# Performance work log

Hardware: AMD Instinct MI355X
Metric: run time of the kernel (lower is better)

## Reference

```python
import jax, jax.numpy as jnp
import numpy as np

# Static configuration (mirrors the list of reconstruction_blocks)
B, F, D, H = 16384, 64, 32, 64
CARDS = ([4, 8, 16, 32] * 8) + [1] * 32  # 32 categorical + 32 numerical features
CMAX = max(CARDS)                         # pad all per-feature output dims to CMAX
TOTAL = sum(CARDS)                        # 512 = concat output width
# flat column indices selecting the valid (unpadded) outputs per feature
_flat = np.concatenate([np.arange(c) + f * CMAX for f, c in enumerate(CARDS)])
FLAT_IDX = jnp.asarray(_flat, dtype=jnp.int32)


def setup_inputs() -> dict:
    key = jax.random.key(0)
    k0, k1, k2 = jax.random.split(key, 3)
    return {
        "inputs": jax.random.normal(k0, (B, F, D), dtype=jnp.float32),
        # per-feature hidden layer: Dense(D -> H)
        "W1": jax.random.normal(k1, (F, D, H), dtype=jnp.float32) / np.float32(np.sqrt(D)),
        "b1": jnp.zeros((F, H), dtype=jnp.float32),
        # per-feature output layer, padded to CMAX columns (only CARDS[f] are used)
        "W2": jax.random.normal(k2, (F, H, CMAX), dtype=jnp.float32) / np.float32(np.sqrt(H)),
        "b2": jnp.zeros((F, CMAX), dtype=jnp.float32),
    }


def reference(inputs, W1, b1, W2, b2):
    # Batched grouped-GEMM over all per-feature MLP blocks at once.
    h = jax.nn.relu(jnp.einsum('bfd,fdh->bfh', inputs, W1) + b1)       # [B,F,H]
    out_pad = jnp.einsum('bfh,fhc->bfc', h, W2) + b2                   # [B,F,CMAX]
    # concat of per-feature outputs (varying widths) == gather of valid columns
    return out_pad.reshape(B, F * CMAX)[:, FLAT_IDX]                   # [B,TOTAL]
```

## Files before the change

### kernel.cpp

```cpp
#include <hip/hip_runtime.h>

typedef __attribute__((ext_vector_type(8))) short short8;
typedef __attribute__((ext_vector_type(4))) float f32x4;

#define DI __device__ __forceinline__

namespace {
constexpr int F_   = 64;
constexpr int D_   = 32;
constexpr int H_   = 64;
constexpr int CM_  = 32;
constexpr int TOT_ = 512;
constexpr int BT_  = 256;
constexpr int NB_  = (16384 / BT_) * F_;
}

DI unsigned short f2bf(float v) {
    __bf16 h = (__bf16)v;
    return __builtin_bit_cast(unsigned short, h);
}

__global__ __launch_bounds__(256)
void recon_kernel(const float* __restrict__ x, const float* __restrict__ W1,
                  const float* __restrict__ b1, const float* __restrict__ W2,
                  const float* __restrict__ b2, float* __restrict__ out)
{
    __shared__ __align__(16) unsigned short w1t[H_ * D_];
    __shared__ __align__(16) unsigned short w2t[CM_ * H_];
    __shared__ __align__(16) unsigned short hb[4][16 * H_];

    const int bid   = blockIdx.x;
    const int f     = (bid >> 3) & 63;
    const int btile = ((bid & 7) << 3) | (bid >> 9);

    const int tid  = threadIdx.x;
    const int lane = tid & 63;
    const int wv   = tid >> 6;
    const int l15  = lane & 15;
    const int kg   = lane >> 4;

    {
        const int e0 = tid * 8;
        const float* W1f = W1 + f * (D_ * H_);
        const float* W2f = W2 + f * (H_ * CM_);
        f32x4 v0 = *(const f32x4*)(W1f + e0);
        f32x4 v1 = *(const f32x4*)(W1f + e0 + 4);
        f32x4 u0 = *(const f32x4*)(W2f + e0);
        f32x4 u1 = *(const f32x4*)(W2f + e0 + 4);
#pragma unroll
        for (int j = 0; j < 8; ++j) {
            int e = e0 + j;
            float v = (j < 4) ? v0[j] : v1[j - 4];
            w1t[(e & 63) * D_ + (e >> 6)] = f2bf(v);
            float u = (j < 4) ? u0[j] : u1[j - 4];
            w2t[(e & 31) * H_ + (e >> 5)] = f2bf(u);
        }
    }
    __syncthreads();

    short8 w1b[4];
#pragma unroll
    for (int nt = 0; nt < 4; ++nt)
        w1b[nt] = *(const short8*)&w1t[(nt * 16 + l15) * D_ + kg * 8];

    short8 w2b[2][2];
#pragma unroll
    for (int nt = 0; nt < 2; ++nt)
#pragma unroll
        for (int ks = 0; ks < 2; ++ks)
            w2b[nt][ks] = *(const short8*)&w2t[(nt * 16 + l15) * H_ + ks * 32 + kg * 8];

    float b1v[4], b2v[2];
#pragma unroll
    for (int nt = 0; nt < 4; ++nt) b1v[nt] = b1[f * H_ + nt * 16 + l15];
#pragma unroll
    for (int nt = 0; nt < 2; ++nt) b2v[nt] = b2[f * CM_ + nt * 16 + l15];

    int card, off;
    if (f < 32) { card = 4 << (f & 3); off = (f >> 2) * 60 + card - 4; }
    else        { card = 1;            off = 480 + (f - 32); }

    unsigned short* hw = hb[wv];
    const f32x4 zero = {0.f, 0.f, 0.f, 0.f};
    const int b0 = btile * BT_ + wv * 64;

#pragma unroll
    for (int t = 0; t < 4; ++t) {
        const int rbase = b0 + t * 16;

        const float* xr = x + (size_t)(rbase + l15) * (F_ * D_) + f * D_ + kg * 8;
        f32x4 a0 = *(const f32x4*)xr;
        f32x4 a1 = *(const f32x4*)(xr + 4);
        short8 af;
#pragma unroll
        for (int j = 0; j < 4; ++j) {
            af[j]     = (short)f2bf(a0[j]);
            af[4 + j] = (short)f2bf(a1[j]);
        }

        f32x4 c1[4];
#pragma unroll
        for (int nt = 0; nt < 4; ++nt)
            c1[nt] = __builtin_amdgcn_mfma_f32_16x16x32_bf16(af, w1b[nt], zero, 0, 0, 0);

#pragma unroll
        for (int nt = 0; nt < 4; ++nt) {
#pragma unroll
            for (int j = 0; j < 4; ++j) {
                int r = kg * 4 + j;
                int c = nt * 16 + l15;
                float v = c1[nt][j] + b1v[nt];
                v = v > 0.f ? v : 0.f;
                int idx = (r * H_ + c) ^ ((r & 7) << 3);
                hw[idx] = f2bf(v);
            }
        }

        short8 ha[2];
#pragma unroll
        for (int ks = 0; ks < 2; ++ks) {
            int idx = (l15 * H_ + ks * 32 + kg * 8) ^ ((l15 & 7) << 3);
            ha[ks] = *(const short8*)&hw[idx];
        }

        f32x4 c2[2];
        c2[0] = __builtin_amdgcn_mfma_f32_16x16x32_bf16(ha[0], w2b[0][0], zero, 0, 0, 0);
        c2[0] = __builtin_amdgcn_mfma_f32_16x16x32_bf16(ha[1], w2b[0][1], c2[0], 0, 0, 0);
        if (card == 32) {
            c2[1] = __builtin_amdgcn_mfma_f32_16x16x32_bf16(ha[0], w2b[1][0], zero, 0, 0, 0);
            c2[1] = __builtin_amdgcn_mfma_f32_16x16x32_bf16(ha[1], w2b[1][1], c2[1], 0, 0, 0);
        }

        const int ntiles = (card == 32) ? 2 : 1;
        for (int nt = 0; nt < ntiles; ++nt) {
            int c = nt * 16 + l15;
            if (c < card) {
                float bias = b2v[nt];
#pragma unroll
                for (int j = 0; j < 4; ++j) {
                    int row = rbase + kg * 4 + j;
                    out[(size_t)row * TOT_ + off + c] = c2[nt][j] + bias;
                }
            }
        }
    }
}

extern "C" void kernel_launch(void* const* d_in, const int* in_sizes, int n_in,
                              void* d_out, int out_size, void* d_ws, size_t ws_size,
                              hipStream_t stream) {
    const float* x  = (const float*)d_in[0];
    const float* W1 = (const float*)d_in[1];
    const float* b1 = (const float*)d_in[2];
    const float* W2 = (const float*)d_in[3];
    const float* b2 = (const float*)d_in[4];
    float* out = (float*)d_out;
    recon_kernel<<<NB_, 256, 0, stream>>>(x, W1, b1, W2, b2, out);
}
```

Baseline: 39.83 us.

## Process eight features per block and stage outputs in LDS for coalesced stores

Each 512-thread block now handles a 64-row tile across eight features, one wave per feature, and loads W1/W2 for all eight into a shared buffer that is reused in phases. All x loads are issued before compute. Per-feature outputs, which are narrow and scattered, are written to an LDS staging tile and then stored to global memory as contiguous 16-byte row segments instead of scattered scalar stores. This aims to cut uncoalesced writes and raise load-level parallelism, at the cost of extra barriers, more LDS per block and fewer blocks.

```diff
diff --git a/kernel.cpp b/kernel.cpp
--- a/kernel.cpp
+++ b/kernel.cpp
@@ -6,13 +6,9 @@
 #define DI __device__ __forceinline__
 
 namespace {
-constexpr int F_   = 64;
-constexpr int D_   = 32;
-constexpr int H_   = 64;
-constexpr int CM_  = 32;
 constexpr int TOT_ = 512;
-constexpr int BT_  = 256;
-constexpr int NB_  = (16384 / BT_) * F_;
+constexpr int XROW = 2048;
+constexpr int NB_  = 2048;
 }
 
 DI unsigned short f2bf(float v) {
@@ -20,82 +16,102 @@
     return __builtin_bit_cast(unsigned short, h);
 }
 
-__global__ __launch_bounds__(256)
+__global__ __launch_bounds__(512)
 void recon_kernel(const float* __restrict__ x, const float* __restrict__ W1,
                   const float* __restrict__ b1, const float* __restrict__ W2,
                   const float* __restrict__ b2, float* __restrict__ out)
 {
-    __shared__ __align__(16) unsigned short w1t[H_ * D_];
-    __shared__ __align__(16) unsigned short w2t[CM_ * H_];
-    __shared__ __align__(16) unsigned short hb[4][16 * H_];
+    __shared__ __align__(16) unsigned short u_sm[24576];
 
-    const int bid   = blockIdx.x;
-    const int f     = (bid >> 3) & 63;
-    const int btile = ((bid & 7) << 3) | (bid >> 9);
+    const int bid     = blockIdx.x;
+    const int xcd     = bid & 7;
+    const int ii      = bid >> 3;
+    const int fg      = ii & 7;
+    const int rowtile = (xcd << 5) | (ii >> 3);
+    const int r0      = rowtile << 6;
 
     const int tid  = threadIdx.x;
     const int lane = tid & 63;
     const int wv   = tid >> 6;
     const int l15  = lane & 15;
     const int kg   = lane >> 4;
+    const int f    = fg * 8 + wv;
 
     {
-        const int e0 = tid * 8;
-        const float* W1f = W1 + f * (D_ * H_);
-        const float* W2f = W2 + f * (H_ * CM_);
-        f32x4 v0 = *(const f32x4*)(W1f + e0);
-        f32x4 v1 = *(const f32x4*)(W1f + e0 + 4);
-        f32x4 u0 = *(const f32x4*)(W2f + e0);
-        f32x4 u1 = *(const f32x4*)(W2f + e0 + 4);
+        const float* src = W1 + (size_t)fg * 8 * 2048;
 #pragma unroll
-        for (int j = 0; j < 8; ++j) {
-            int e = e0 + j;
-            float v = (j < 4) ? v0[j] : v1[j - 4];
-            w1t[(e & 63) * D_ + (e >> 6)] = f2bf(v);
-            float u = (j < 4) ? u0[j] : u1[j - 4];
-            w2t[(e & 31) * H_ + (e >> 5)] = f2bf(u);
+        for (int it = 0; it < 4; ++it) {
+            int e0 = (it * 512 + tid) * 8;
+            f32x4 v0 = *(const f32x4*)(src + e0);
+            f32x4 v1 = *(const f32x4*)(src + e0 + 4);
+#pragma unroll
+            for (int j = 0; j < 8; ++j) {
+                int e = e0 + j, f8 = e >> 11, r = e & 2047;
+                float v = (j < 4) ? v0[j] : v1[j - 4];
+                u_sm[(f8 << 11) | ((r & 63) << 5) | (r >> 6)] = f2bf(v);
+            }
         }
     }
     __syncthreads();
-
     short8 w1b[4];
 #pragma unroll
     for (int nt = 0; nt < 4; ++nt)
-        w1b[nt] = *(const short8*)&w1t[(nt * 16 + l15) * D_ + kg * 8];
+        w1b[nt] = *(const short8*)&u_sm[wv * 2048 + (nt * 16 + l15) * 32 + kg * 8];
+    __syncthreads();
 
+    {
+        const float* src = W2 + (size_t)fg * 8 * 2048;
+#pragma unroll
+        for (int it = 0; it < 4; ++it) {
+            int e0 = (it * 512 + tid) * 8;
+            f32x4 v0 = *(const f32x4*)(src + e0);
+            f32x4 v1 = *(const f32x4*)(src + e0 + 4);
+#pragma unroll
+            for (int j = 0; j < 8; ++j) {
+                int e = e0 + j, f8 = e >> 11, r = e & 2047;
+                float v = (j < 4) ? v0[j] : v1[j - 4];
+                u_sm[(f8 << 11) | ((r & 31) << 6) | (r >> 5)] = f2bf(v);
+            }
+        }
+    }
+    __syncthreads();
     short8 w2b[2][2];
 #pragma unroll
     for (int nt = 0; nt < 2; ++nt)
 #pragma unroll
         for (int ks = 0; ks < 2; ++ks)
-            w2b[nt][ks] = *(const short8*)&w2t[(nt * 16 + l15) * H_ + ks * 32 + kg * 8];
+            w2b[nt][ks] = *(const short8*)&u_sm[wv * 2048 + (nt * 16 + l15) * 64 + ks * 32 + kg * 8];
+    __syncthreads();
 
     float b1v[4], b2v[2];
 #pragma unroll
-    for (int nt = 0; nt < 4; ++nt) b1v[nt] = b1[f * H_ + nt * 16 + l15];
+    for (int nt = 0; nt < 4; ++nt) b1v[nt] = b1[f * 64 + nt * 16 + l15];
 #pragma unroll
-    for (int nt = 0; nt < 2; ++nt) b2v[nt] = b2[f * CM_ + nt * 16 + l15];
+    for (int nt = 0; nt < 2; ++nt) b2v[nt] = b2[f * 32 + nt * 16 + l15];
 
-    int card, off;
-    if (f < 32) { card = 4 << (f & 3); off = (f >> 2) * 60 + card - 4; }
-    else        { card = 1;            off = 480 + (f - 32); }
+    int card, offl;
+    if (f < 32) { card = 4 << (wv & 3); offl = (wv >> 2) * 60 + card - 4; }
+    else        { card = 1;             offl = wv; }
 
-    unsigned short* hw = hb[wv];
+    unsigned short* hw = u_sm + 16384 + wv * 1024;
+    float* outl = (float*)u_sm;
     const f32x4 zero = {0.f, 0.f, 0.f, 0.f};
-    const int b0 = btile * BT_ + wv * 64;
+
+    f32x4 xa[4][2];
+#pragma unroll
+    for (int t = 0; t < 4; ++t) {
+        const float* xr = x + (size_t)(r0 + t * 16 + l15) * XROW + f * 32 + kg * 8;
+        xa[t][0] = *(const f32x4*)xr;
+        xa[t][1] = *(const f32x4*)(xr + 4);
+    }
 
 #pragma unroll
     for (int t = 0; t < 4; ++t) {
-        const int rbase = b0 + t * 16;
-
-        const float* xr = x + (size_t)(rbase + l15) * (F_ * D_) + f * D_ + kg * 8;
-        f32x4 a0 = *(const f32x4*)xr;
-        f32x4 a1 = *(const f32x4*)(xr + 4);
         short8 af;
 #pragma unroll
         for (int j = 0; j < 4; ++j) {
-            af[j]     = (short)f2bf(a0[j]);
-            af[4 + j] = (short)f2bf(a1[j]);
+            af[j]     = (short)f2bf(xa[t][0][j]);
+            af[4 + j] = (short)f2bf(xa[t][1][j]);
         }
 
         f32x4 c1[4];
@@ -111,17 +127,14 @@
                 int c = nt * 16 + l15;
                 float v = c1[nt][j] + b1v[nt];
                 v = v > 0.f ? v : 0.f;
-                int idx = (r * H_ + c) ^ ((r & 7) << 3);
-                hw[idx] = f2bf(v);
+                hw[(r * 64 + c) ^ ((r & 7) << 3)] = f2bf(v);
             }
         }
 
         short8 ha[2];
 #pragma unroll
-        for (int ks = 0; ks < 2; ++ks) {
-            int idx = (l15 * H_ + ks * 32 + kg * 8) ^ ((l15 & 7) << 3);
-            ha[ks] = *(const short8*)&hw[idx];
-        }
+        for (int ks = 0; ks < 2; ++ks)
+            ha[ks] = *(const short8*)&hw[(l15 * 64 + ks * 32 + kg * 8) ^ ((l15 & 7) << 3)];
 
         f32x4 c2[2];
         c2[0] = __builtin_amdgcn_mfma_f32_16x16x32_bf16(ha[0], w2b[0][0], zero, 0, 0, 0);
@@ -133,15 +146,31 @@
 
         const int ntiles = (card == 32) ? 2 : 1;
         for (int nt = 0; nt < ntiles; ++nt) {
-            int c = nt * 16 + l15;
-            if (c < card) {
+            if (l15 < card) {
                 float bias = b2v[nt];
 #pragma unroll
-                for (int j = 0; j < 4; ++j) {
-                    int row = rbase + kg * 4 + j;
-                    out[(size_t)row * TOT_ + off + c] = c2[nt][j] + bias;
-                }
+                for (int j = 0; j < 4; ++j)
+                    outl[(t * 16 + kg * 4 + j) * 124 + offl + nt * 16 + l15] = c2[nt][j] + bias;
             }
+        }
+    }
+    __syncthreads();
+
+    if (fg < 4) {
+#pragma unroll
+        for (int it = 0; it < 4; ++it) {
+            int c = tid + it * 512;
+            if (c < 1920) {
+                int row = c / 30, q = c - row * 30;
+                f32x4 v = *(const f32x4*)&outl[row * 124 + q * 4];
+                *(f32x4*)(out + (size_t)(r0 + row) * TOT_ + fg * 120 + q * 4) = v;
+            }
+        }
+    } else {
+        if (tid < 128) {
+            int row = tid >> 1, half = tid & 1;
+            f32x4 v = *(const f32x4*)&outl[row * 124 + half * 4];
+            *(f32x4*)(out + (size_t)(r0 + row) * TOT_ + 480 + (fg - 4) * 8 + half * 4) = v;
         }
     }
 }
@@ -155,5 +184,5 @@
     const float* W2 = (const float*)d_in[3];
     const float* b2 = (const float*)d_in[4];
     float* out = (float*)d_out;
-    recon_kernel<<<NB_, 256, 0, stream>>>(x, W1, b1, W2, b2, out);
+    recon_kernel<<<NB_, 512, 0, stream>>>(x, W1, b1, W2, b2, out);
 }
```

Measured after the change: 53.94 us. +35.4%, slower.

## Transpose MFMA operands for vectorized stores and prefetch all x tiles upfront

Applied to the files above, without the earlier changes.

Swaps the A/B operands of both MFMA stages so each lane holds four consecutive output columns for one row. This allows the hidden activations to be written to LDS as 4-wide vectors and the final outputs to be stored to global memory as float4 instead of scalar strided stores. Bias loads become vector loads to match the new layout. All four x row tiles are loaded into registers before any compute to raise memory-level parallelism. The cost is higher register pressure, plus output offsets that must stay 16-byte aligned for the vector stores.

```diff
diff --git a/kernel.cpp b/kernel.cpp
--- a/kernel.cpp
+++ b/kernel.cpp
@@ -2,17 +2,15 @@
 
 typedef __attribute__((ext_vector_type(8))) short short8;
 typedef __attribute__((ext_vector_type(4))) float f32x4;
+typedef __attribute__((ext_vector_type(4))) unsigned short u16x4;
 
 #define DI __device__ __forceinline__
 
 namespace {
-constexpr int F_   = 64;
-constexpr int D_   = 32;
-constexpr int H_   = 64;
-constexpr int CM_  = 32;
 constexpr int TOT_ = 512;
+constexpr int XROW = 2048;
 constexpr int BT_  = 256;
-constexpr int NB_  = (16384 / BT_) * F_;
+constexpr int NB_  = (16384 / BT_) * 64;
 }
 
 DI unsigned short f2bf(float v) {
@@ -25,9 +23,9 @@
                   const float* __restrict__ b1, const float* __restrict__ W2,
                   const float* __restrict__ b2, float* __restrict__ out)
 {
-    __shared__ __align__(16) unsigned short w1t[H_ * D_];
-    __shared__ __align__(16) unsigned short w2t[CM_ * H_];
-    __shared__ __align__(16) unsigned short hb[4][16 * H_];
+    __shared__ __align__(16) unsigned short w1t[64 * 32];
+    __shared__ __align__(16) unsigned short w2t[32 * 64];
+    __shared__ __align__(16) unsigned short hb[4][16 * 64];
 
     const int bid   = blockIdx.x;
     const int f     = (bid >> 3) & 63;
@@ -38,11 +36,12 @@
     const int wv   = tid >> 6;
     const int l15  = lane & 15;
     const int kg   = lane >> 4;
+    const int swz  = (l15 & 7) << 3;
 
     {
         const int e0 = tid * 8;
-        const float* W1f = W1 + f * (D_ * H_);
-        const float* W2f = W2 + f * (H_ * CM_);
+        const float* W1f = W1 + f * 2048;
+        const float* W2f = W2 + f * 2048;
         f32x4 v0 = *(const f32x4*)(W1f + e0);
         f32x4 v1 = *(const f32x4*)(W1f + e0 + 4);
         f32x4 u0 = *(const f32x4*)(W2f + e0);
@@ -51,9 +50,9 @@
         for (int j = 0; j < 8; ++j) {
             int e = e0 + j;
             float v = (j < 4) ? v0[j] : v1[j - 4];
-            w1t[(e & 63) * D_ + (e >> 6)] = f2bf(v);
+            w1t[(e & 63) * 32 + (e >> 6)] = f2bf(v);
             float u = (j < 4) ? u0[j] : u1[j - 4];
-            w2t[(e & 31) * H_ + (e >> 5)] = f2bf(u);
+            w2t[(e & 31) * 64 + (e >> 5)] = f2bf(u);
         }
     }
     __syncthreads();
@@ -61,20 +60,20 @@
     short8 w1b[4];
 #pragma unroll
     for (int nt = 0; nt < 4; ++nt)
-        w1b[nt] = *(const short8*)&w1t[(nt * 16 + l15) * D_ + kg * 8];
+        w1b[nt] = *(const short8*)&w1t[(nt * 16 + l15) * 32 + kg * 8];
 
     short8 w2b[2][2];
 #pragma unroll
     for (int nt = 0; nt < 2; ++nt)
 #pragma unroll
         for (int ks = 0; ks < 2; ++ks)
-            w2b[nt][ks] = *(const short8*)&w2t[(nt * 16 + l15) * H_ + ks * 32 + kg * 8];
+            w2b[nt][ks] = *(const short8*)&w2t[(nt * 16 + l15) * 64 + ks * 32 + kg * 8];
 
-    float b1v[4], b2v[2];
+    f32x4 b1q[4], b2q[2];
 #pragma unroll
-    for (int nt = 0; nt < 4; ++nt) b1v[nt] = b1[f * H_ + nt * 16 + l15];
+    for (int nt = 0; nt < 4; ++nt) b1q[nt] = *(const f32x4*)(b1 + f * 64 + nt * 16 + kg * 4);
 #pragma unroll
-    for (int nt = 0; nt < 2; ++nt) b2v[nt] = b2[f * CM_ + nt * 16 + l15];
+    for (int nt = 0; nt < 2; ++nt) b2q[nt] = *(const f32x4*)(b2 + f * 32 + nt * 16 + kg * 4);
 
     int card, off;
     if (f < 32) { card = 4 << (f & 3); off = (f >> 2) * 60 + card - 4; }
@@ -84,64 +83,66 @@
     const f32x4 zero = {0.f, 0.f, 0.f, 0.f};
     const int b0 = btile * BT_ + wv * 64;
 
+    f32x4 xa[4][2];
 #pragma unroll
     for (int t = 0; t < 4; ++t) {
-        const int rbase = b0 + t * 16;
+        const float* xr = x + (size_t)(b0 + t * 16 + l15) * XROW + f * 32 + kg * 8;
+        xa[t][0] = *(const f32x4*)xr;
+        xa[t][1] = *(const f32x4*)(xr + 4);
+    }
 
-        const float* xr = x + (size_t)(rbase + l15) * (F_ * D_) + f * D_ + kg * 8;
-        f32x4 a0 = *(const f32x4*)xr;
-        f32x4 a1 = *(const f32x4*)(xr + 4);
+#pragma unroll
+    for (int t = 0; t < 4; ++t) {
         short8 af;
 #pragma unroll
         for (int j = 0; j < 4; ++j) {
-            af[j]     = (short)f2bf(a0[j]);
-            af[4 + j] = (short)f2bf(a1[j]);
+            af[j]     = (short)f2bf(xa[t][0][j]);
+            af[4 + j] = (short)f2bf(xa[t][1][j]);
         }
 
         f32x4 c1[4];
 #pragma unroll
         for (int nt = 0; nt < 4; ++nt)
-            c1[nt] = __builtin_amdgcn_mfma_f32_16x16x32_bf16(af, w1b[nt], zero, 0, 0, 0);
+            c1[nt] = __builtin_amdgcn_mfma_f32_16x16x32_bf16(w1b[nt], af, zero, 0, 0, 0);
 
 #pragma unroll
         for (int nt = 0; nt < 4; ++nt) {
+            u16x4 hv;
 #pragma unroll
             for (int j = 0; j < 4; ++j) {
-                int r = kg * 4 + j;
-                int c = nt * 16 + l15;
-                float v = c1[nt][j] + b1v[nt];
-                v = v > 0.f ? v : 0.f;
-                int idx = (r * H_ + c) ^ ((r & 7) << 3);
-                hw[idx] = f2bf(v);
+                float v = c1[nt][j] + b1q[nt][j];
+                hv[j] = f2bf(v > 0.f ? v : 0.f);
             }
+            *(u16x4*)&hw[(l15 * 64 + nt * 16 + kg * 4) ^ swz] = hv;
         }
 
         short8 ha[2];
 #pragma unroll
-        for (int ks = 0; ks < 2; ++ks) {
-            int idx = (l15 * H_ + ks * 32 + kg * 8) ^ ((l15 & 7) << 3);
-            ha[ks] = *(const short8*)&hw[idx];
+        for (int ks = 0; ks < 2; ++ks)
+            ha[ks] = *(const short8*)&hw[(l15 * 64 + ks * 32 + kg * 8) ^ swz];
+
+        f32x4 c2[2];
+        c2[0] = __builtin_amdgcn_mfma_f32_16x16x32_bf16(w2b[0][0], ha[0], zero, 0, 0, 0);
+        c2[0] = __builtin_amdgcn_mfma_f32_16x16x32_bf16(w2b[0][1], ha[1], c2[0], 0, 0, 0);
+        if (card == 32) {
+            c2[1] = __builtin_amdgcn_mfma_f32_16x16x32_bf16(w2b[1][0], ha[0], zero, 0, 0, 0);
+            c2[1] = __builtin_amdgcn_mfma_f32_16x16x32_bf16(w2b[1][1], ha[1], c2[1], 0, 0, 0);
         }
 
-        f32x4 c2[2];
-        c2[0] = __builtin_amdgcn_mfma_f32_16x16x32_bf16(ha[0], w2b[0][0], zero, 0, 0, 0);
-        c2[0] = __builtin_amdgcn_mfma_f32_16x16x32_bf16(ha[1], w2b[0][1], c2[0], 0, 0, 0);
-        if (card == 32) {
-            c2[1] = __builtin_amdgcn_mfma_f32_16x16x32_bf16(ha[0], w2b[1][0], zero, 0, 0, 0);
-            c2[1] = __builtin_amdgcn_mfma_f32_16x16x32_bf16(ha[1], w2b[1][1], c2[1], 0, 0, 0);
-        }
-
-        const int ntiles = (card == 32) ? 2 : 1;
-        for (int nt = 0; nt < ntiles; ++nt) {
-            int c = nt * 16 + l15;
-            if (c < card) {
-                float bias = b2v[nt];
+        const int row = b0 + t * 16 + l15;
+        if (card > 1) {
+            const int ntiles = (card == 32) ? 2 : 1;
+            for (int nt = 0; nt < ntiles; ++nt) {
+                if (kg * 4 < card - nt * 16) {
+                    f32x4 v;
 #pragma unroll
-                for (int j = 0; j < 4; ++j) {
-                    int row = rbase + kg * 4 + j;
-                    out[(size_t)row * TOT_ + off + c] = c2[nt][j] + bias;
+                    for (int j = 0; j < 4; ++j) v[j] = c2[nt][j] + b2q[nt][j];
+                    *(f32x4*)(out + (size_t)row * TOT_ + off + nt * 16 + kg * 4) = v;
                 }
             }
+        } else {
+            if (kg == 0)
+                out[(size_t)row * TOT_ + off] = c2[0][0] + b2q[0][0];
         }
     }
 }
```

After: 39.61 us. About the same (-0.6%).
